# Kernel tuning notes

Measured on AMD Instinct MI355X. Metric: run time of the kernel, lower is better.

The kernel has to match this reference:

```python
import jax, jax.numpy as jnp
import numpy as np

M = 512          # feature_dim
NH = 8           # num_heads
FFN = 2048       # ffn_hidden_dim
NMOD = 4         # modalities (seq len for attention)
EPS = 1e-5


def setup_inputs() -> dict:
    key = jax.random.key(0)
    ks = jax.random.split(key, 16)
    B, H = 64, 256
    s = 0.02
    return {
        "x_image": jax.random.normal(ks[0], (B, H, M), jnp.float32),
        "x_radar": jax.random.normal(ks[1], (B, H, M), jnp.float32),
        "x_lidar": jax.random.normal(ks[2], (B, H, M), jnp.float32),
        "x_gps":   jax.random.normal(ks[3], (B, H, M), jnp.float32),
        # nn.MultiheadAttention params (torch layout: weight is (out,in))
        "in_proj_w": jax.random.normal(ks[4], (3 * M, M), jnp.float32) * s,
        "in_proj_b": jnp.zeros((3 * M,), jnp.float32),
        "out_proj_w": jax.random.normal(ks[5], (M, M), jnp.float32) * s,
        "out_proj_b": jnp.zeros((M,), jnp.float32),
        "ln1_g": jnp.ones((M,), jnp.float32),
        "ln1_b": jnp.zeros((M,), jnp.float32),
        "w1": jax.random.normal(ks[6], (FFN, M), jnp.float32) * s,
        "b1": jnp.zeros((FFN,), jnp.float32),
        "w2": jax.random.normal(ks[7], (M, FFN), jnp.float32) * s,
        "b2": jnp.zeros((M,), jnp.float32),
        "ln2_g": jnp.ones((M,), jnp.float32),
        "ln2_b": jnpp if False else jnp.zeros((M,), jnp.float32),
    }


def _layernorm(x, g, b):
    mu = jnp.mean(x, axis=-1, keepdims=True)
    var = jnp.mean((x - mu) ** 2, axis=-1, keepdims=True)
    return (x - mu) * jax.lax.rsqrt(var + EPS) * g + b


def _forward(x_image, x_radar, x_lidar, x_gps,
             in_proj_w, in_proj_b, out_proj_w, out_proj_b,
             ln1_g, ln1_b, w1, b1, w2, b2, ln2_g, ln2_b):
    B, H, _ = x_image.shape
    # F: (B*H, NMOD, M) -- fold batch and time; per-t loop is independent
    F = jnp.stack([x_image, x_radar, x_lidar, x_gps], axis=2).reshape(B * H, NMOD, M)
    qkv = F @ in_proj_w.T + in_proj_b              # (N, NMOD, 3M)
    q, k, v = jnp.split(qkv, 3, axis=-1)
    dh = M // NH
    def heads(t):  # (N, NMOD, M) -> (N, NH, NMOD, dh)
        return t.reshape(-1, NMOD, NH, dh).transpose(0, 2, 1, 3)
    qh, kh, vh = heads(q), heads(k), heads(v)
    scores = jnp.einsum("bhsd,bhtd->bhst", qh, kh) / np.sqrt(dh).astype(np.float32)
    attn = jax.nn.softmax(scores, axis=-1)
    o = jnp.einsum("bhst,bhtd->bhsd", attn, vh)
    o = o.transpose(0, 2, 1, 3).reshape(-1, NMOD, M)
    attn_out = o @ out_proj_w.T + out_proj_b
    h1 = _layernorm(F + attn_out, ln1_g, ln1_b)    # (N, NMOD, M)
    agg = h1.sum(axis=1)                            # (N, M)
    ffn = jax.nn.gelu(agg @ w1.T + b1, approximate=False) @ w2.T + b2
    z = _layernorm(agg + ffn, ln2_g, ln2_b)
    return z.reshape(B, H, M)


def reference(x_image, x_radar, x_lidar, x_gps,
              in_proj_w, in_proj_b, out_proj_w, out_proj_b,
              ln1_g, ln1_b, w1, b1, w2, b2, ln2_g, ln2_b):
    return _forward(x_image, x_radar, x_lidar, x_gps,
                    in_proj_w, in_proj_b, out_proj_w, out_proj_b,
                    ln1_g, ln1_b, w1, b1, w2, b2, ln2_g, ln2_b)
```

## Files before the change

### kernel.cpp

```cpp
#include <hip/hip_runtime.h>
#include <hip/hip_bf16.h>


typedef __attribute__((ext_vector_type(8))) short s16x8;
typedef __attribute__((ext_vector_type(4))) float f32x4;

__device__ __forceinline__ unsigned short f2bf(float f) {
  unsigned int u = __float_as_uint(f);
  u += 0x7fffu + ((u >> 16) & 1u);
  return (unsigned short)(u >> 16);
}
__device__ __forceinline__ float bf2f(unsigned short s) {
  return __uint_as_float(((unsigned int)s) << 16);
}
__device__ __forceinline__ f32x4 mfma16(s16x8 a, s16x8 b, f32x4 c) {
  return __builtin_amdgcn_mfma_f32_16x16x32_bf16(a, b, c, 0, 0, 0);
}
__device__ __forceinline__ int swz(int row, int bir) {
  return row * 128 + ((((row) & 7) << 4) ^ bir);
}
__device__ __forceinline__ int qkswz(int row, int c) {
  return row * 128 + ((((c >> 3) ^ (row & 7)) << 4)) + (c & 7) * 2;
}
__device__ __forceinline__ int vtswz(int d, int row) {
  return d * 256 + ((((row >> 3) ^ (d & 7)) << 4)) + (row & 7) * 2;
}
__device__ __forceinline__ int pwswz(int row, int c) {
  return row * 64 + ((((c >> 3) ^ (row & 3)) << 4)) + (c & 7) * 2;
}
__device__ __forceinline__ int vtoff(int r, int c) {
  return r * 1024 + ((c * 2) ^ ((r & 7) << 4));
}
__device__ __forceinline__ void gl_lds16(const void* g, void* l) {
  __builtin_amdgcn_global_load_lds(
      (const __attribute__((address_space(1))) unsigned int*)g,
      (__attribute__((address_space(3))) unsigned int*)l, 16, 0, 0);
}

__global__ void pack_kernel(const float* __restrict__ wqkv, const float* __restrict__ wout,
                            const float* __restrict__ w1, const float* __restrict__ w2,
                            const float* __restrict__ x0, const float* __restrict__ x1,
                            const float* __restrict__ x2, const float* __restrict__ x3,
                            unsigned short* __restrict__ o_wqkv, unsigned short* __restrict__ o_wout,
                            unsigned short* __restrict__ o_w1, unsigned short* __restrict__ o_w2,
                            unsigned short* __restrict__ o_x4) {
  const long c0 = 196608, c1 = 262144, c2 = 524288, c3 = 786432, c4 = 9175040;
  for (long v = (long)blockIdx.x * blockDim.x + threadIdx.x; v < c4;
       v += (long)gridDim.x * blockDim.x) {
    const float* src;
    unsigned short* dst;
    if (v < c0) { src = wqkv + v * 4; dst = o_wqkv + v * 4; }
    else if (v < c1) { long u = v - c0; src = wout + u * 4; dst = o_wout + u * 4; }
    else if (v < c2) { long u = v - c1; src = w1 + u * 4; dst = o_w1 + u * 4; }
    else if (v < c3) { long u = v - c2; src = w2 + u * 4; dst = o_w2 + u * 4; }
    else {
      long u = v - c3; long e = u * 4; long r = e >> 9; int i = (int)(e & 511);
      int s = (int)(r & 3); long n = r >> 2;
      const float* xs = (s == 0) ? x0 : (s == 1) ? x1 : (s == 2) ? x2 : x3;
      src = xs + n * 512 + i; dst = o_x4 + e;
    }
    float4 f = *reinterpret_cast<const float4*>(src);
    ushort4 hb;
    hb.x = f2bf(f.x); hb.y = f2bf(f.y); hb.z = f2bf(f.z); hb.w = f2bf(f.w);
    *reinterpret_cast<ushort4*>(dst) = hb;
  }
}

__launch_bounds__(256, 2)
__global__ void qkv_attn_kernel(const unsigned short* __restrict__ x4,
                                const unsigned short* __restrict__ wqkv,
                                const float* __restrict__ in_b,
                                unsigned short* __restrict__ o_out) {
  const int wg = blockIdx.x;
  const int slot = wg >> 3, xcd = wg & 7;
  const int tb = ((slot >> 3) << 3) | xcd;
  const int h = slot & 7;
  const int tid = threadIdx.x, lane = tid & 63, w = tid >> 6;
  const int wm = w >> 1, wn = w & 1;

  __shared__ __align__(16) unsigned char smem[49152];
  unsigned short* aT = (unsigned short*)smem;
  unsigned short* bT = (unsigned short*)(smem + 16384);
  unsigned short* Qs = (unsigned short*)smem;
  unsigned short* Ks = (unsigned short*)(smem + 16384);
  unsigned short* Vt = (unsigned short*)(smem + 32768);
  unsigned short* Pw = (unsigned short*)smem;
  unsigned short* outT = (unsigned short*)(smem + 16384);

  f32x4 acc[4][6];
#pragma unroll
  for (int i = 0; i < 4; ++i)
#pragma unroll
    for (int j = 0; j < 6; ++j) acc[i][j] = (f32x4){0.f, 0.f, 0.f, 0.f};

  const long rowBase = (long)tb * 128;

  for (int kk = 0; kk < 8; ++kk) {
    const int k0 = kk * 64;
#pragma unroll
    for (int it = 0; it < 4; ++it) {
      int cid = tid + it * 256, lr = cid >> 3, c8 = cid & 7;
      s16x8 v = *(const s16x8*)(x4 + (rowBase + lr) * 512 + k0 + c8 * 8);
      *(s16x8*)((unsigned char*)aT + swz(lr, c8 * 16)) = v;
    }
#pragma unroll
    for (int it = 0; it < 6; ++it) {
      int cid = tid + it * 256, bc = cid >> 3, c8 = cid & 7;
      int wrow = (bc < 64) ? (h * 64 + bc)
                : (bc < 128) ? (512 + h * 64 + (bc - 64))
                             : (1024 + h * 64 + (bc - 128));
      s16x8 v = *(const s16x8*)(wqkv + (long)wrow * 512 + k0 + c8 * 8);
      *(s16x8*)((unsigned char*)bT + swz(bc, c8 * 16)) = v;
    }
    __syncthreads();
#pragma unroll
    for (int k2 = 0; k2 < 2; ++k2) {
      s16x8 af[4], bfr[6];
      const int bir = k2 * 64 + ((lane >> 4) << 4);
#pragma unroll
      for (int mi = 0; mi < 4; ++mi) {
        int row = wm * 64 + mi * 16 + (lane & 15);
        af[mi] = *(const s16x8*)((unsigned char*)aT + swz(row, bir));
      }
#pragma unroll
      for (int ni = 0; ni < 6; ++ni) {
        int col = wn * 96 + ni * 16 + (lane & 15);
        bfr[ni] = *(const s16x8*)((unsigned char*)bT + swz(col, bir));
      }
#pragma unroll
      for (int mi = 0; mi < 4; ++mi)
#pragma unroll
        for (int ni = 0; ni < 6; ++ni)
          acc[mi][ni] = mfma16(af[mi], bfr[ni], acc[mi][ni]);
    }
    __syncthreads();
  }

#pragma unroll
  for (int mi = 0; mi < 4; ++mi)
#pragma unroll
    for (int ni = 0; ni < 6; ++ni) {
      int col = wn * 96 + ni * 16 + (lane & 15);
      int wb = (col < 64) ? (h * 64 + col)
             : (col < 128) ? (512 + h * 64 + (col - 64))
                           : (1024 + h * 64 + (col - 128));
      float bias = in_b[wb];
      int row0 = wm * 64 + mi * 16 + ((lane >> 4) << 2);
#pragma unroll
      for (int r = 0; r < 4; ++r) {
        int row = row0 + r;
        unsigned short hv = f2bf(acc[mi][ni][r] + bias);
        if (col < 64)
          *(unsigned short*)((unsigned char*)Qs + qkswz(row, col)) = hv;
        else if (col < 128)
          *(unsigned short*)((unsigned char*)Ks + qkswz(row, col - 64)) = hv;
        else
          *(unsigned short*)((unsigned char*)Vt + vtswz(col - 128, row)) = hv;
      }
    }
  __syncthreads();

  f32x4 sacc[2];
#pragma unroll
  for (int i2 = 0; i2 < 2; ++i2) {
    int ti = w * 2 + i2;
    int qrow = ti * 16 + (lane & 15);
    int bir = (lane >> 4) << 4;
    s16x8 qa0 = *(const s16x8*)((unsigned char*)Qs + swz(qrow, bir));
    s16x8 qa1 = *(const s16x8*)((unsigned char*)Qs + swz(qrow, 64 + bir));
    s16x8 ka0 = *(const s16x8*)((unsigned char*)Ks + swz(qrow, bir));
    s16x8 ka1 = *(const s16x8*)((unsigned char*)Ks + swz(qrow, 64 + bir));
    f32x4 s = (f32x4){0.f, 0.f, 0.f, 0.f};
    s = mfma16(qa0, ka0, s);
    s = mfma16(qa1, ka1, s);
    sacc[i2] = s;
  }
  __syncthreads();
  {
    s16x8 z = (s16x8){0, 0, 0, 0, 0, 0, 0, 0};
    ((s16x8*)Pw)[tid] = z;
    ((s16x8*)Pw)[tid + 256] = z;
  }
  __syncthreads();

  const bool rel = ((lane & 15) >> 2) == (lane >> 4);
#pragma unroll
  for (int i2 = 0; i2 < 2; ++i2) {
    int ti = w * 2 + i2;
#pragma unroll
    for (int r = 0; r < 4; ++r) {
      float sc = sacc[i2][r] * 0.125f;
      float m = fmaxf(sc, __shfl_xor(sc, 1));
      m = fmaxf(m, __shfl_xor(m, 2));
      float e = __expf(sc - m);
      float su = e + __shfl_xor(e, 1);
      su = su + __shfl_xor(su, 2);
      float p = e / su;
      if (rel) {
        int row = ti * 16 + ((lane >> 4) << 2) + r;
        int cl = (((row >> 2) & 7) << 2) + (lane & 3);
        *(unsigned short*)((unsigned char*)Pw + pwswz(row, cl)) = f2bf(p);
      }
    }
  }
  __syncthreads();

#pragma unroll
  for (int i2 = 0; i2 < 2; ++i2) {
    int ti = w * 2 + i2;
    int arow = ti * 16 + (lane & 15);
    s16x8 pa = *(const s16x8*)((unsigned char*)Pw + arow * 64 +
                               ((((lane >> 4) ^ (arow & 3)) << 4)));
    f32x4 pv4[4];
#pragma unroll
    for (int n = 0; n < 4; ++n) {
      int d = n * 16 + (lane & 15);
      int gran = ((ti >> 1) << 2) + (lane >> 4);
      s16x8 vb = *(const s16x8*)((unsigned char*)Vt + d * 256 +
                                 (((gran ^ (d & 7)) << 4)));
      pv4[n] = mfma16(pa, vb, (f32x4){0.f, 0.f, 0.f, 0.f});
    }
#pragma unroll
    for (int n = 0; n < 4; ++n) {
      int d = n * 16 + (lane & 15);
      int row0 = ti * 16 + ((lane >> 4) << 2);
#pragma unroll
      for (int r = 0; r < 4; ++r)
        *(unsigned short*)((unsigned char*)outT + qkswz(row0 + r, d)) =
            f2bf(pv4[n][r]);
    }
  }
  __syncthreads();
#pragma unroll
  for (int j = 0; j < 4; ++j) {
    int c = j * 256 + tid;
    int row = c >> 3, ch = c & 7;
    s16x8 v = *(const s16x8*)((unsigned char*)outT + qkswz(row, ch * 8));
    *(s16x8*)(o_out + (rowBase + row) * 512 + h * 64 + ch * 8) = v;
  }
}

__launch_bounds__(256)
__global__ void outproj_ln1_kernel(const unsigned short* __restrict__ o_in,
                                   const unsigned short* __restrict__ wout,
                                   const float* __restrict__ out_b,
                                   const unsigned short* __restrict__ x4,
                                   const float* __restrict__ ln1_g, const float* __restrict__ ln1_b,
                                   float* __restrict__ agg_f, unsigned short* __restrict__ agg_b) {
  const int tb = blockIdx.x;
  const int tid = threadIdx.x, lane = tid & 63, w = tid >> 6;
  __shared__ __align__(16) unsigned char smem[53504];
  unsigned short* vt = (unsigned short*)smem;
  unsigned short* aT = (unsigned short*)(smem + 32768);
  unsigned short* bT = (unsigned short*)(smem + 36864);
  float* stats = (float*)(smem + 53248);
  const long rowBase = (long)tb * 32;

  for (int ns = 0; ns < 4; ++ns) {
    f32x4 acc[2][2];
#pragma unroll
    for (int i = 0; i < 2; ++i)
#pragma unroll
      for (int j = 0; j < 2; ++j) acc[i][j] = (f32x4){0.f, 0.f, 0.f, 0.f};
    for (int kk = 0; kk < 8; ++kk) {
      const int k0 = kk * 64;
      {
        int lr = tid >> 3, c8 = tid & 7;
        s16x8 v = *(const s16x8*)(o_in + (rowBase + lr) * 512 + k0 + c8 * 8);
        *(s16x8*)((unsigned char*)aT + swz(lr, c8 * 16)) = v;
      }
#pragma unroll
      for (int it = 0; it < 4; ++it) {
        int cid = tid + it * 256, bc = cid >> 3, c8 = cid & 7;
        s16x8 v = *(const s16x8*)(wout + (long)(ns * 128 + bc) * 512 + k0 + c8 * 8);
        *(s16x8*)((unsigned char*)bT + swz(bc, c8 * 16)) = v;
      }
      __syncthreads();
#pragma unroll
      for (int k2 = 0; k2 < 2; ++k2) {
        s16x8 af[2], bfr[2];
        const int bir = k2 * 64 + ((lane >> 4) << 4);
#pragma unroll
        for (int mi = 0; mi < 2; ++mi) {
          int row = mi * 16 + (lane & 15);
          af[mi] = *(const s16x8*)((unsigned char*)aT + swz(row, bir));
        }
#pragma unroll
        for (int ni = 0; ni < 2; ++ni) {
          int col = w * 32 + ni * 16 + (lane & 15);
          bfr[ni] = *(const s16x8*)((unsigned char*)bT + swz(col, bir));
        }
#pragma unroll
        for (int mi = 0; mi < 2; ++mi)
#pragma unroll
          for (int ni = 0; ni < 2; ++ni)
            acc[mi][ni] = mfma16(af[mi], bfr[ni], acc[mi][ni]);
      }
      __syncthreads();
    }
#pragma unroll
    for (int mi = 0; mi < 2; ++mi)
#pragma unroll
      for (int ni = 0; ni < 2; ++ni) {
        int gcol = ns * 128 + w * 32 + ni * 16 + (lane & 15);
        float bias = out_b[gcol];
        int row0 = mi * 16 + ((lane >> 4) << 2);
#pragma unroll
        for (int r = 0; r < 4; ++r) {
          int rr = row0 + r;
          float F = bf2f(x4[(rowBase + rr) * 512 + gcol]);
          *(unsigned short*)((unsigned char*)vt + vtoff(rr, gcol)) =
              f2bf(acc[mi][ni][r] + bias + F);
        }
      }
  }
  __syncthreads();
  {
    int wv = tid >> 6, ln = tid & 63;
    for (int i = 0; i < 8; ++i) {
      int r = wv * 8 + i;
      s16x8 v8 = *(const s16x8*)((unsigned char*)vt + vtoff(r, ln * 8));
      float sum = 0.f, sq = 0.f;
#pragma unroll
      for (int d = 0; d < 8; ++d) {
        float v = bf2f((unsigned short)v8[d]);
        sum += v; sq += v * v;
      }
#pragma unroll
      for (int off = 1; off < 64; off <<= 1) {
        sum += __shfl_xor(sum, off); sq += __shfl_xor(sq, off);
      }
      if (ln == 0) {
        float mu = sum * (1.f / 512.f);
        float var = sq * (1.f / 512.f) - mu * mu;
        stats[r * 2] = mu;
        stats[r * 2 + 1] = rsqrtf(var + 1e-5f);
      }
    }
  }
  __syncthreads();
  for (int it = 0; it < 2; ++it) {
    int ci = tid + it * 256;
    int tok = ci >> 6, c0 = (ci & 63) * 8;
    long gtok = (long)tb * 8 + tok;
    float a[8] = {0.f, 0.f, 0.f, 0.f, 0.f, 0.f, 0.f, 0.f};
#pragma unroll
    for (int s = 0; s < 4; ++s) {
      int r = tok * 4 + s;
      s16x8 v8 = *(const s16x8*)((unsigned char*)vt + vtoff(r, c0));
      float mu = stats[r * 2], is = stats[r * 2 + 1];
#pragma unroll
      for (int d = 0; d < 8; ++d) a[d] += (bf2f((unsigned short)v8[d]) - mu) * is;
    }
    float4 g0 = *(const float4*)(ln1_g + c0);
    float4 g1 = *(const float4*)(ln1_g + c0 + 4);
    float4 b0 = *(const float4*)(ln1_b + c0);
    float4 b1 = *(const float4*)(ln1_b + c0 + 4);
    float ov[8];
    ov[0] = g0.x * a[0] + 4.f * b0.x; ov[1] = g0.y * a[1] + 4.f * b0.y;
    ov[2] = g0.z * a[2] + 4.f * b0.z; ov[3] = g0.w * a[3] + 4.f * b0.w;
    ov[4] = g1.x * a[4] + 4.f * b1.x; ov[5] = g1.y * a[5] + 4.f * b1.y;
    ov[6] = g1.z * a[6] + 4.f * b1.z; ov[7] = g1.w * a[7] + 4.f * b1.w;
    *(float4*)(agg_f + gtok * 512 + c0) = (float4){ov[0], ov[1], ov[2], ov[3]};
    *(float4*)(agg_f + gtok * 512 + c0 + 4) = (float4){ov[4], ov[5], ov[6], ov[7]};
    s16x8 ab;
#pragma unroll
    for (int d = 0; d < 8; ++d) ab[d] = (short)f2bf(ov[d]);
    *(s16x8*)(agg_b + gtok * 512 + c0) = ab;
  }
}

__launch_bounds__(256)
__global__ void ffn1_kernel(const unsigned short* __restrict__ aggb,
                            const unsigned short* __restrict__ w1b,
                            const float* __restrict__ b1,
                            unsigned short* __restrict__ hidden) {
  const int wg = blockIdx.x;
  const int slot = wg >> 3, xcd = wg & 7;
  const int by = ((slot >> 4) << 3) | xcd;
  const int bx = slot & 15;
  const int tid = threadIdx.x, lane = tid & 63, w = tid >> 6;
  const int wm = w >> 1, wn = w & 1;
  __shared__ __align__(16) unsigned char smem[32768];
  unsigned short* aT = (unsigned short*)smem;
  unsigned short* bT = (unsigned short*)(smem + 16384);
  f32x4 acc[4][4];
#pragma unroll
  for (int i = 0; i < 4; ++i)
#pragma unroll
    for (int j = 0; j < 4; ++j) acc[i][j] = (f32x4){0.f, 0.f, 0.f, 0.f};
  const long rowBase = (long)by * 128;
  const long colBase = (long)bx * 128;
  const int loff = ((lane >> 3) * 512) + (((lane & 7) ^ (lane >> 3)) * 8);
  for (int kk = 0; kk < 8; ++kk) {
    const int k0 = kk * 64;
#pragma unroll
    for (int it = 0; it < 4; ++it) {
      int c = w * 4 + it;
      gl_lds16(aggb + (rowBase + c * 8) * 512 + k0 + loff, aT + c * 512);
    }
#pragma unroll
    for (int it = 0; it < 4; ++it) {
      int c = w * 4 + it;
      gl_lds16(w1b + (colBase + c * 8) * 512 + k0 + loff, bT + c * 512);
    }
    __syncthreads();
#pragma unroll
    for (int k2 = 0; k2 < 2; ++k2) {
      s16x8 af[4], bfr[4];
      const int bir = k2 * 64 + ((lane >> 4) << 4);
#pragma unroll
      for (int mi = 0; mi < 4; ++mi) {
        int row = wm * 64 + mi * 16 + (lane & 15);
        af[mi] = *(const s16x8*)((unsigned char*)aT + swz(row, bir));
      }
#pragma unroll
      for (int ni = 0; ni < 4; ++ni) {
        int col = wn * 64 + ni * 16 + (lane & 15);
        bfr[ni] = *(const s16x8*)((unsigned char*)bT + swz(col, bir));
      }
#pragma unroll
      for (int mi = 0; mi < 4; ++mi)
#pragma unroll
        for (int ni = 0; ni < 4; ++ni)
          acc[mi][ni] = mfma16(af[mi], bfr[ni], acc[mi][ni]);
    }
    __syncthreads();
  }
#pragma unroll
  for (int mi = 0; mi < 4; ++mi)
#pragma unroll
    for (int ni = 0; ni < 4; ++ni) {
      long gcol = colBase + wn * 64 + ni * 16 + (lane & 15);
      float bias = b1[gcol];
      int row0 = wm * 64 + mi * 16 + ((lane >> 4) << 2);
#pragma unroll
      for (int r = 0; r < 4; ++r) {
        float x = acc[mi][ni][r] + bias;
        float g = 0.5f * x * (1.f + erff(x * 0.70710678118f));
        hidden[(rowBase + row0 + r) * 2048 + gcol] = f2bf(g);
      }
    }
}

__launch_bounds__(256)
__global__ void ffn2_kernel(const unsigned short* __restrict__ hidden,
                            const unsigned short* __restrict__ w2b,
                            const float* __restrict__ b2,
                            const float* __restrict__ agg_f,
                            float* __restrict__ ffn2s) {
  const int wg = blockIdx.x;
  const int slot = wg >> 3, xcd = wg & 7;
  const int by = ((slot >> 2) << 3) | xcd;
  const int bx = slot & 3;
  const int tid = threadIdx.x, lane = tid & 63, w = tid >> 6;
  const int wm = w >> 1, wn = w & 1;
  __shared__ __align__(16) unsigned char smem[32768];
  unsigned short* aT = (unsigned short*)smem;
  unsigned short* bT = (unsigned short*)(smem + 16384);
  f32x4 acc[4][4];
#pragma unroll
  for (int i = 0; i < 4; ++i)
#pragma unroll
    for (int j = 0; j < 4; ++j) acc[i][j] = (f32x4){0.f, 0.f, 0.f, 0.f};
  const long rowBase = (long)by * 128;
  const long colBase = (long)bx * 128;
  const int loff2k = ((lane >> 3) * 2048) + (((lane & 7) ^ (lane >> 3)) * 8);
  for (int kk = 0; kk < 32; ++kk) {
    const int k0 = kk * 64;
#pragma unroll
    for (int it = 0; it < 4; ++it) {
      int c = w * 4 + it;
      gl_lds16(hidden + (rowBase + c * 8) * 2048 + k0 + loff2k, aT + c * 512);
    }
#pragma unroll
    for (int it = 0; it < 4; ++it) {
      int c = w * 4 + it;
      gl_lds16(w2b + (colBase + c * 8) * 2048 + k0 + loff2k, bT + c * 512);
    }
    __syncthreads();
#pragma unroll
    for (int k2 = 0; k2 < 2; ++k2) {
      s16x8 af[4], bfr[4];
      const int bir = k2 * 64 + ((lane >> 4) << 4);
#pragma unroll
      for (int mi = 0; mi < 4; ++mi) {
        int row = wm * 64 + mi * 16 + (lane & 15);
        af[mi] = *(const s16x8*)((unsigned char*)aT + swz(row, bir));
      }
#pragma unroll
      for (int ni = 0; ni < 4; ++ni) {
        int col = wn * 64 + ni * 16 + (lane & 15);
        bfr[ni] = *(const s16x8*)((unsigned char*)bT + swz(col, bir));
      }
#pragma unroll
      for (int mi = 0; mi < 4; ++mi)
#pragma unroll
        for (int ni = 0; ni < 4; ++ni)
          acc[mi][ni] = mfma16(af[mi], bfr[ni], acc[mi][ni]);
    }
    __syncthreads();
  }
#pragma unroll
  for (int mi = 0; mi < 4; ++mi)
#pragma unroll
    for (int ni = 0; ni < 4; ++ni) {
      long gcol = colBase + wn * 64 + ni * 16 + (lane & 15);
      float bias = b2[gcol];
      int row0 = wm * 64 + mi * 16 + ((lane >> 4) << 2);
#pragma unroll
      for (int r = 0; r < 4; ++r) {
        long grow = rowBase + row0 + r;
        ffn2s[grow * 512 + gcol] = acc[mi][ni][r] + bias + agg_f[grow * 512 + gcol];
      }
    }
}

__launch_bounds__(256)
__global__ void ln2_kernel(const float* __restrict__ ffn2s,
                           const float* __restrict__ ln2_g,
                           const float* __restrict__ ln2_b,
                           float* __restrict__ out) {
  const int tb = blockIdx.x;
  const int lane = threadIdx.x & 63, wv = threadIdx.x >> 6;
  const int c0 = lane * 8;
  float4 g0 = *(const float4*)(ln2_g + c0);
  float4 g1 = *(const float4*)(ln2_g + c0 + 4);
  float4 b0 = *(const float4*)(ln2_b + c0);
  float4 b1 = *(const float4*)(ln2_b + c0 + 4);
#pragma unroll
  for (int i = 0; i < 4; ++i) {
    long row = (long)tb * 16 + wv * 4 + i;
    const float* src = ffn2s + row * 512 + c0;
    float4 a = *(const float4*)src;
    float4 c = *(const float4*)(src + 4);
    float sum = a.x + a.y + a.z + a.w + c.x + c.y + c.z + c.w;
    float sq = a.x * a.x + a.y * a.y + a.z * a.z + a.w * a.w +
               c.x * c.x + c.y * c.y + c.z * c.z + c.w * c.w;
#pragma unroll
    for (int off = 1; off < 64; off <<= 1) {
      sum += __shfl_xor(sum, off); sq += __shfl_xor(sq, off);
    }
    float mu = sum * (1.f / 512.f);
    float is = rsqrtf(sq * (1.f / 512.f) - mu * mu + 1e-5f);
    float* dst = out + row * 512 + c0;
    *(float4*)dst = (float4){(a.x - mu) * is * g0.x + b0.x, (a.y - mu) * is * g0.y + b0.y,
                             (a.z - mu) * is * g0.z + b0.z, (a.w - mu) * is * g0.w + b0.w};
    *(float4*)(dst + 4) = (float4){(c.x - mu) * is * g1.x + b1.x, (c.y - mu) * is * g1.y + b1.y,
                                   (c.z - mu) * is * g1.z + b1.z, (c.w - mu) * is * g1.w + b1.w};
  }
}

extern "C" void kernel_launch(void* const* d_in, const int* in_sizes, int n_in,
                              void* d_out, int out_size, void* d_ws, size_t ws_size,
                              hipStream_t stream) {
  (void)in_sizes; (void)n_in; (void)out_size;
  const float* x0 = (const float*)d_in[0];
  const float* x1 = (const float*)d_in[1];
  const float* x2 = (const float*)d_in[2];
  const float* x3 = (const float*)d_in[3];
  const float* in_w = (const float*)d_in[4];
  const float* in_b = (const float*)d_in[5];
  const float* out_w = (const float*)d_in[6];
  const float* out_b = (const float*)d_in[7];
  const float* ln1_g = (const float*)d_in[8];
  const float* ln1_b = (const float*)d_in[9];
  const float* w1 = (const float*)d_in[10];
  const float* b1 = (const float*)d_in[11];
  const float* w2 = (const float*)d_in[12];
  const float* b2 = (const float*)d_in[13];
  const float* ln2_g = (const float*)d_in[14];
  const float* ln2_b = (const float*)d_in[15];
  float* out = (float*)d_out;

  unsigned char* ws = (unsigned char*)d_ws;
  if (ws_size < 190840832u) return;
  unsigned short* wqkv_b = (unsigned short*)(ws + 0);
  unsigned short* wout_b = (unsigned short*)(ws + 1572864);
  unsigned short* w1_b = (unsigned short*)(ws + 2097152);
  unsigned short* w2_b = (unsigned short*)(ws + 4194304);
  unsigned short* x4 = (unsigned short*)(ws + 6291456);
  unsigned short* o_buf = (unsigned short*)(ws + 73400320);
  float* agg_f = (float*)(ws + 140509184);
  unsigned short* agg_b = (unsigned short*)(ws + 174063616);
  unsigned short* hidden = o_buf;
  float* ffn2s = (float*)(ws + 6291456);

  pack_kernel<<<2048, 256, 0, stream>>>(in_w, out_w, w1, w2, x0, x1, x2, x3,
                                        wqkv_b, wout_b, w1_b, w2_b, x4);
  qkv_attn_kernel<<<4096, 256, 0, stream>>>(x4, wqkv_b, in_b, o_buf);
  outproj_ln1_kernel<<<2048, 256, 0, stream>>>(o_buf, wout_b, out_b, x4,
                                               ln1_g, ln1_b, agg_f, agg_b);
  ffn1_kernel<<<2048, 256, 0, stream>>>(agg_b, w1_b, b1, hidden);
  ffn2_kernel<<<512, 256, 0, stream>>>(hidden, w2_b, b2, agg_f, ffn2s);
  ln2_kernel<<<1024, 256, 0, stream>>>(ffn2s, ln2_g, ln2_b, out);
}
```

Measured before the change: 420.8 us.

## Fuse input bf16 packing into QKV kernel and halve its row tile

Removes the separate pass that packs the four fp32 modality inputs into an interleaved bf16 buffer. The QKV/attention kernel now reads fp32 inputs directly and converts them while staging into LDS. The out-projection residual now reads fp32 inputs as well. The QKV kernel tile shrinks from 128 to 64 rows, with LDS cut to 32 KB, twice the blocks and occupancy raised to 3. This drops a 67 MB write plus reread, but every head's block now re-reads and re-converts fp32 activations, doubling input traffic per head, and weight tiles are reused across fewer rows.

```diff
diff --git a/kernel.cpp b/kernel.cpp
--- a/kernel.cpp
+++ b/kernel.cpp
@@ -22,8 +22,8 @@
 __device__ __forceinline__ int qkswz(int row, int c) {
   return row * 128 + ((((c >> 3) ^ (row & 7)) << 4)) + (c & 7) * 2;
 }
-__device__ __forceinline__ int vtswz(int d, int row) {
-  return d * 256 + ((((row >> 3) ^ (d & 7)) << 4)) + (row & 7) * 2;
+__device__ __forceinline__ int vtswz64(int d, int row) {
+  return d * 128 + ((((row >> 3) ^ (d & 7)) << 4)) + (row & 7) * 2;
 }
 __device__ __forceinline__ int pwswz(int row, int c) {
   return row * 64 + ((((c >> 3) ^ (row & 3)) << 4)) + (c & 7) * 2;
@@ -37,28 +37,19 @@
       (__attribute__((address_space(3))) unsigned int*)l, 16, 0, 0);
 }
 
-__global__ void pack_kernel(const float* __restrict__ wqkv, const float* __restrict__ wout,
-                            const float* __restrict__ w1, const float* __restrict__ w2,
-                            const float* __restrict__ x0, const float* __restrict__ x1,
-                            const float* __restrict__ x2, const float* __restrict__ x3,
-                            unsigned short* __restrict__ o_wqkv, unsigned short* __restrict__ o_wout,
-                            unsigned short* __restrict__ o_w1, unsigned short* __restrict__ o_w2,
-                            unsigned short* __restrict__ o_x4) {
-  const long c0 = 196608, c1 = 262144, c2 = 524288, c3 = 786432, c4 = 9175040;
-  for (long v = (long)blockIdx.x * blockDim.x + threadIdx.x; v < c4;
+__global__ void pack_w_kernel(const float* __restrict__ wqkv, const float* __restrict__ wout,
+                              const float* __restrict__ w1, const float* __restrict__ w2,
+                              unsigned short* __restrict__ o_wqkv, unsigned short* __restrict__ o_wout,
+                              unsigned short* __restrict__ o_w1, unsigned short* __restrict__ o_w2) {
+  const long c0 = 196608, c1 = 262144, c2 = 524288, c3 = 786432;
+  for (long v = (long)blockIdx.x * blockDim.x + threadIdx.x; v < c3;
        v += (long)gridDim.x * blockDim.x) {
     const float* src;
     unsigned short* dst;
     if (v < c0) { src = wqkv + v * 4; dst = o_wqkv + v * 4; }
     else if (v < c1) { long u = v - c0; src = wout + u * 4; dst = o_wout + u * 4; }
     else if (v < c2) { long u = v - c1; src = w1 + u * 4; dst = o_w1 + u * 4; }
-    else if (v < c3) { long u = v - c2; src = w2 + u * 4; dst = o_w2 + u * 4; }
-    else {
-      long u = v - c3; long e = u * 4; long r = e >> 9; int i = (int)(e & 511);
-      int s = (int)(r & 3); long n = r >> 2;
-      const float* xs = (s == 0) ? x0 : (s == 1) ? x1 : (s == 2) ? x2 : x3;
-      src = xs + n * 512 + i; dst = o_x4 + e;
-    }
+    else { long u = v - c2; src = w2 + u * 4; dst = o_w2 + u * 4; }
     float4 f = *reinterpret_cast<const float4*>(src);
     ushort4 hb;
     hb.x = f2bf(f.x); hb.y = f2bf(f.y); hb.z = f2bf(f.z); hb.w = f2bf(f.w);
@@ -66,8 +57,9 @@
   }
 }
 
-__launch_bounds__(256, 2)
-__global__ void qkv_attn_kernel(const unsigned short* __restrict__ x4,
+__launch_bounds__(256, 3)
+__global__ void qkv_attn_kernel(const float* __restrict__ x0, const float* __restrict__ x1,
+                                const float* __restrict__ x2, const float* __restrict__ x3,
                                 const unsigned short* __restrict__ wqkv,
                                 const float* __restrict__ in_b,
                                 unsigned short* __restrict__ o_out) {
@@ -78,29 +70,40 @@
   const int tid = threadIdx.x, lane = tid & 63, w = tid >> 6;
   const int wm = w >> 1, wn = w & 1;
 
-  __shared__ __align__(16) unsigned char smem[49152];
+  __shared__ __align__(16) unsigned char smem[32768];
   unsigned short* aT = (unsigned short*)smem;
-  unsigned short* bT = (unsigned short*)(smem + 16384);
+  unsigned short* bT = (unsigned short*)(smem + 8192);
   unsigned short* Qs = (unsigned short*)smem;
-  unsigned short* Ks = (unsigned short*)(smem + 16384);
-  unsigned short* Vt = (unsigned short*)(smem + 32768);
-  unsigned short* Pw = (unsigned short*)smem;
-  unsigned short* outT = (unsigned short*)(smem + 16384);
-
-  f32x4 acc[4][6];
-#pragma unroll
-  for (int i = 0; i < 4; ++i)
+  unsigned short* Ks = (unsigned short*)(smem + 8192);
+  unsigned short* Vt = (unsigned short*)(smem + 16384);
+  unsigned short* Pw = (unsigned short*)(smem + 24576);
+  unsigned short* outT = (unsigned short*)smem;
+
+  f32x4 acc[2][6];
+#pragma unroll
+  for (int i = 0; i < 2; ++i)
 #pragma unroll
     for (int j = 0; j < 6; ++j) acc[i][j] = (f32x4){0.f, 0.f, 0.f, 0.f};
 
-  const long rowBase = (long)tb * 128;
+  const long rowBase = (long)tb * 64;
+  const long tokBase = (long)tb * 16;
 
   for (int kk = 0; kk < 8; ++kk) {
     const int k0 = kk * 64;
 #pragma unroll
-    for (int it = 0; it < 4; ++it) {
+    for (int it = 0; it < 2; ++it) {
       int cid = tid + it * 256, lr = cid >> 3, c8 = cid & 7;
-      s16x8 v = *(const s16x8*)(x4 + (rowBase + lr) * 512 + k0 + c8 * 8);
+      int s = lr & 3;
+      long n = tokBase + (lr >> 2);
+      const float* src = (s == 0) ? x0 : (s == 1) ? x1 : (s == 2) ? x2 : x3;
+      src += n * 512 + k0 + c8 * 8;
+      float4 f0 = *(const float4*)src;
+      float4 f1 = *(const float4*)(src + 4);
+      s16x8 v;
+      v[0] = (short)f2bf(f0.x); v[1] = (short)f2bf(f0.y);
+      v[2] = (short)f2bf(f0.z); v[3] = (short)f2bf(f0.w);
+      v[4] = (short)f2bf(f1.x); v[5] = (short)f2bf(f1.y);
+      v[6] = (short)f2bf(f1.z); v[7] = (short)f2bf(f1.w);
       *(s16x8*)((unsigned char*)aT + swz(lr, c8 * 16)) = v;
     }
 #pragma unroll
@@ -115,11 +118,11 @@
     __syncthreads();
 #pragma unroll
     for (int k2 = 0; k2 < 2; ++k2) {
-      s16x8 af[4], bfr[6];
+      s16x8 af[2], bfr[6];
       const int bir = k2 * 64 + ((lane >> 4) << 4);
 #pragma unroll
-      for (int mi = 0; mi < 4; ++mi) {
-        int row = wm * 64 + mi * 16 + (lane & 15);
+      for (int mi = 0; mi < 2; ++mi) {
+        int row = wm * 32 + mi * 16 + (lane & 15);
         af[mi] = *(const s16x8*)((unsigned char*)aT + swz(row, bir));
       }
 #pragma unroll
@@ -128,7 +131,7 @@
         bfr[ni] = *(const s16x8*)((unsigned char*)bT + swz(col, bir));
       }
 #pragma unroll
-      for (int mi = 0; mi < 4; ++mi)
+      for (int mi = 0; mi < 2; ++mi)
 #pragma unroll
         for (int ni = 0; ni < 6; ++ni)
           acc[mi][ni] = mfma16(af[mi], bfr[ni], acc[mi][ni]);
@@ -137,7 +140,7 @@
   }
 
 #pragma unroll
-  for (int mi = 0; mi < 4; ++mi)
+  for (int mi = 0; mi < 2; ++mi)
 #pragma unroll
     for (int ni = 0; ni < 6; ++ni) {
       int col = wn * 96 + ni * 16 + (lane & 15);
@@ -145,7 +148,7 @@
              : (col < 128) ? (512 + h * 64 + (col - 64))
                            : (1024 + h * 64 + (col - 128));
       float bias = in_b[wb];
-      int row0 = wm * 64 + mi * 16 + ((lane >> 4) << 2);
+      int row0 = wm * 32 + mi * 16 + ((lane >> 4) << 2);
 #pragma unroll
       for (int r = 0; r < 4; ++r) {
         int row = row0 + r;
@@ -155,15 +158,14 @@
         else if (col < 128)
           *(unsigned short*)((unsigned char*)Ks + qkswz(row, col - 64)) = hv;
         else
-          *(unsigned short*)((unsigned char*)Vt + vtswz(col - 128, row)) = hv;
-      }
-    }
-  __syncthreads();
-
-  f32x4 sacc[2];
-#pragma unroll
-  for (int i2 = 0; i2 < 2; ++i2) {
-    int ti = w * 2 + i2;
+          *(unsigned short*)((unsigned char*)Vt + vtswz64(col - 128, row)) = hv;
+      }
+    }
+  __syncthreads();
+
+  f32x4 sacc;
+  {
+    int ti = w;
     int qrow = ti * 16 + (lane & 15);
     int bir = (lane >> 4) << 4;
     s16x8 qa0 = *(const s16x8*)((unsigned char*)Qs + swz(qrow, bir));
@@ -173,23 +175,21 @@
     f32x4 s = (f32x4){0.f, 0.f, 0.f, 0.f};
     s = mfma16(qa0, ka0, s);
     s = mfma16(qa1, ka1, s);
-    sacc[i2] = s;
+    sacc = s;
   }
   __syncthreads();
   {
     s16x8 z = (s16x8){0, 0, 0, 0, 0, 0, 0, 0};
     ((s16x8*)Pw)[tid] = z;
-    ((s16x8*)Pw)[tid + 256] = z;
   }
   __syncthreads();
 
   const bool rel = ((lane & 15) >> 2) == (lane >> 4);
-#pragma unroll
-  for (int i2 = 0; i2 < 2; ++i2) {
-    int ti = w * 2 + i2;
+  {
+    int ti = w;
 #pragma unroll
     for (int r = 0; r < 4; ++r) {
-      float sc = sacc[i2][r] * 0.125f;
+      float sc = sacc[r] * 0.125f;
       float m = fmaxf(sc, __shfl_xor(sc, 1));
       m = fmaxf(m, __shfl_xor(m, 2));
       float e = __expf(sc - m);
@@ -205,9 +205,8 @@
   }
   __syncthreads();
 
-#pragma unroll
-  for (int i2 = 0; i2 < 2; ++i2) {
-    int ti = w * 2 + i2;
+  {
+    int ti = w;
     int arow = ti * 16 + (lane & 15);
     s16x8 pa = *(const s16x8*)((unsigned char*)Pw + arow * 64 +
                                ((((lane >> 4) ^ (arow & 3)) << 4)));
@@ -216,7 +215,7 @@
     for (int n = 0; n < 4; ++n) {
       int d = n * 16 + (lane & 15);
       int gran = ((ti >> 1) << 2) + (lane >> 4);
-      s16x8 vb = *(const s16x8*)((unsigned char*)Vt + d * 256 +
+      s16x8 vb = *(const s16x8*)((unsigned char*)Vt + d * 128 +
                                  (((gran ^ (d & 7)) << 4)));
       pv4[n] = mfma16(pa, vb, (f32x4){0.f, 0.f, 0.f, 0.f});
     }
@@ -232,7 +231,7 @@
   }
   __syncthreads();
 #pragma unroll
-  for (int j = 0; j < 4; ++j) {
+  for (int j = 0; j < 2; ++j) {
     int c = j * 256 + tid;
     int row = c >> 3, ch = c & 7;
     s16x8 v = *(const s16x8*)((unsigned char*)outT + qkswz(row, ch * 8));
@@ -244,7 +243,8 @@
 __global__ void outproj_ln1_kernel(const unsigned short* __restrict__ o_in,
                                    const unsigned short* __restrict__ wout,
                                    const float* __restrict__ out_b,
-                                   const unsigned short* __restrict__ x4,
+                                   const float* __restrict__ x0, const float* __restrict__ x1,
+                                   const float* __restrict__ x2, const float* __restrict__ x3,
                                    const float* __restrict__ ln1_g, const float* __restrict__ ln1_b,
                                    float* __restrict__ agg_f, unsigned short* __restrict__ agg_b) {
   const int tb = blockIdx.x;
@@ -255,6 +255,7 @@
   unsigned short* bT = (unsigned short*)(smem + 36864);
   float* stats = (float*)(smem + 53248);
   const long rowBase = (long)tb * 32;
+  const float* xs[4] = {x0, x1, x2, x3};
 
   for (int ns = 0; ns < 4; ++ns) {
     f32x4 acc[2][2];
@@ -308,7 +309,9 @@
 #pragma unroll
         for (int r = 0; r < 4; ++r) {
           int rr = row0 + r;
-          float F = bf2f(x4[(rowBase + rr) * 512 + gcol]);
+          long grow = rowBase + rr;
+          int s = (int)(grow & 3); long n = grow >> 2;
+          float F = xs[s][n * 512 + gcol];
           *(unsigned short*)((unsigned char*)vt + vtoff(rr, gcol)) =
               f2bf(acc[mi][ni][r] + bias + F);
         }
@@ -579,17 +582,16 @@
   unsigned short* wout_b = (unsigned short*)(ws + 1572864);
   unsigned short* w1_b = (unsigned short*)(ws + 2097152);
   unsigned short* w2_b = (unsigned short*)(ws + 4194304);
-  unsigned short* x4 = (unsigned short*)(ws + 6291456);
+  float* ffn2s = (float*)(ws + 6291456);
   unsigned short* o_buf = (unsigned short*)(ws + 73400320);
   float* agg_f = (float*)(ws + 140509184);
   unsigned short* agg_b = (unsigned short*)(ws + 174063616);
   unsigned short* hidden = o_buf;
-  float* ffn2s = (float*)(ws + 6291456);
-
-  pack_kernel<<<2048, 256, 0, stream>>>(in_w, out_w, w1, w2, x0, x1, x2, x3,
-                                        wqkv_b, wout_b, w1_b, w2_b, x4);
-  qkv_attn_kernel<<<4096, 256, 0, stream>>>(x4, wqkv_b, in_b, o_buf);
-  outproj_ln1_kernel<<<2048, 256, 0, stream>>>(o_buf, wout_b, out_b, x4,
+
+  pack_w_kernel<<<1024, 256, 0, stream>>>(in_w, out_w, w1, w2,
+                                          wqkv_b, wout_b, w1_b, w2_b);
+  qkv_attn_kernel<<<8192, 256, 0, stream>>>(x0, x1, x2, x3, wqkv_b, in_b, o_buf);
+  outproj_ln1_kernel<<<2048, 256, 0, stream>>>(o_buf, wout_b, out_b, x0, x1, x2, x3,
                                                ln1_g, ln1_b, agg_f, agg_b);
   ffn1_kernel<<<2048, 256, 0, stream>>>(agg_b, w1_b, b1, hidden);
   ffn2_kernel<<<512, 256, 0, stream>>>(hidden, w2_b, b2, agg_f, ffn2s);
```

Result: slower. 460.0 us (+9.3%).
